# Performance work log

Hardware: AMD Instinct MI355X
Metric: run time of the kernel (lower is better)

## Reference

```python
import jax, jax.numpy as jnp
import numpy as np

B, N, IN_DIM, HID = 8, 4096, 256, 256


def setup_inputs() -> dict:
    key = jax.random.key(0)
    ks = jax.random.split(key, 7)
    s_in = 1.0 / np.sqrt(IN_DIM)
    return {
        "x": jax.random.normal(ks[0], (B, N, IN_DIM), dtype=jnp.float32),
        "Wq": jax.random.uniform(ks[1], (IN_DIM, HID), jnp.float32, -s_in, s_in),
        "bq": jax.random.uniform(ks[2], (HID,), jnp.float32, -s_in, s_in),
        "Wk": jax.random.uniform(ks[3], (IN_DIM, HID), jnp.float32, -s_in, s_in),
        "bk": jax.random.uniform(ks[4], (HID,), jnp.float32, -s_in, s_in),
        "Wv": jax.random.uniform(ks[5], (IN_DIM, HID), jnp.float32, -s_in, s_in),
        "bv": jax.random.uniform(ks[6], (HID,), jnp.float32, -s_in, s_in),
    }


def reference(x, Wq, bq, Wk, bk, Wv, bv):
    # x: [B, N, in_dim]
    Q = jnp.einsum("bnd,dh->bnh", x, Wq) + bq  # [B, N, H]
    K = jnp.einsum("bnd,dh->bnh", x, Wk) + bk
    V = jnp.einsum("bnd,dh->bnh", x, Wv) + bv
    scale = 1.0 / jnp.sqrt(jnp.asarray(K.shape[-1], dtype=x.dtype))
    scores = jnp.einsum("bqh,bkh->bqk", Q, K) * scale  # [B, N, N]
    attn = jax.nn.softmax(scores, axis=-1)
    out = jnp.einsum("bqk,bkh->bqh", attn, V)  # [B, N, H]
    return out.mean(axis=1)  # [B, H]
```

## Files before the change

kernel.cpp:

```cpp
#include <hip/hip_runtime.h>
#include <hip/hip_bf16.h>


#define NTOK 4096
#define HDIM 256
#define NBATCH 8
#define SCALE 0.0625f

typedef __attribute__((ext_vector_type(8))) short short8_t;
typedef __attribute__((ext_vector_type(16))) float f32x16;

__device__ __forceinline__ unsigned short f2bf(float f) {
    unsigned u = __float_as_uint(f);
    u += 0x7fff + ((u >> 16) & 1);
    return (unsigned short)(u >> 16);
}

#define MFMA(a, b, c) __builtin_amdgcn_mfma_f32_32x32x16_bf16(a, b, c, 0, 0, 0)

__device__ __forceinline__ void async_cp16(const void* g, void* l) {
    __builtin_amdgcn_global_load_lds((const __attribute__((address_space(1))) void*)g,
                                     (__attribute__((address_space(3))) void*)l, 16, 0, 0);
}

__device__ __forceinline__ void stage_swz(unsigned short* lds, const unsigned short* src,
                                          int row0, int dbase, int w, int l) {
#pragma unroll
    for (int i = 0; i < 4; ++i) {
        int rloc = w * 32 + i * 8 + (l >> 3);
        int u = (l & 7) ^ (l >> 3);
        const unsigned short* g = src + (size_t)(row0 + rloc) * HDIM + dbase + u * 8;
        unsigned short* d = lds + (w * 32 + i * 8) * 64;
        async_cp16(g, d);
    }
}

__device__ __forceinline__ short8_t frd(const unsigned short* lds, int rb, int lo, int u) {
    return *(const short8_t*)(lds + ((rb * 32 + lo) * 8 + (u ^ (lo & 7))) * 8);
}

__device__ __forceinline__ void stage64(unsigned short* lds, const unsigned short* src,
                                        int w, const int* soff) {
#pragma unroll
    for (int j = 0; j < 4; ++j)
        async_cp16(src + soff[j], lds + (size_t)(w * 4 + j) * 512);
}

__device__ __forceinline__ short8_t krd(const unsigned short* lds, int r, int u) {
    int dc = u >> 3, uu = u & 7;
    return *(const short8_t*)(lds + ((dc * 64 + r) * 8 + (uu ^ (r & 7))) * 8);
}

__global__ void zero_kernel(float* __restrict__ w, float* __restrict__ l, float* __restrict__ out) {
    int i = blockIdx.x * 256 + threadIdx.x;
    w[i] = 0.f;
    l[i] = 0.f;
    if (i < NBATCH * HDIM) out[i] = 0.f;
}

__global__ void convert_x(const float* __restrict__ x, unsigned short* __restrict__ xbf) {
    int i = (blockIdx.x * 256 + threadIdx.x) * 4;
    float4 v = *(const float4*)(x + i);
    ushort4 o;
    o.x = f2bf(v.x); o.y = f2bf(v.y); o.z = f2bf(v.z); o.w = f2bf(v.w);
    *(ushort4*)(xbf + i) = o;
}

__global__ void convert_wt(const float* __restrict__ Wq, const float* __restrict__ Wk,
                           const float* __restrict__ Wv, unsigned short* __restrict__ Wt) {
    int z = blockIdx.y;
    const float* W = (z == 0) ? Wq : (z == 1) ? Wk : Wv;
    unsigned short* o = Wt + z * 65536;
    int n = threadIdx.x;
    for (int kk = 0; kk < 32; ++kk) {
        int k = blockIdx.x * 32 + kk;
        o[n * 256 + k] = f2bf(W[k * 256 + n]);
    }
}

__global__ __launch_bounds__(256) void qkv_mfma(const unsigned short* __restrict__ xbf,
                                                const unsigned short* __restrict__ Wt,
                                                const float* __restrict__ bq, const float* __restrict__ bk,
                                                const float* __restrict__ bv,
                                                unsigned short* __restrict__ Qbf,
                                                unsigned short* __restrict__ Kbf,
                                                float* __restrict__ Vf) {
    const int z = blockIdx.z;
    const unsigned short* Wz = Wt + z * 65536;
    const float* bias = (z == 0) ? bq : (z == 1) ? bk : bv;
    const int m0 = blockIdx.x * 128, n0 = blockIdx.y * 128;
    const int t = threadIdx.x, w = t >> 6, l = t & 63, lo = l & 31, hi = l >> 5;
    const int rm = (w & 1) * 2, rn = (w >> 1) * 2;

    __shared__ __align__(16) char smem[32768];
    unsigned short* Xb = (unsigned short*)smem;
    unsigned short* Wb = (unsigned short*)(smem + 16384);

    f32x16 acc[2][2];
#pragma unroll
    for (int a = 0; a < 2; ++a)
#pragma unroll
        for (int c = 0; c < 2; ++c)
#pragma unroll
            for (int r = 0; r < 16; ++r) acc[a][c][r] = 0.f;

    for (int dc = 0; dc < 4; ++dc) {
        __syncthreads();
        stage_swz(Xb, xbf, m0, dc * 64, w, l);
        stage_swz(Wb, Wz, n0, dc * 64, w, l);
        __syncthreads();
#pragma unroll
        for (int ks = 0; ks < 4; ++ks) {
            int u = ks * 2 + hi;
            short8_t a0 = frd(Xb, rm + 0, lo, u);
            short8_t a1 = frd(Xb, rm + 1, lo, u);
            short8_t b0 = frd(Wb, rn + 0, lo, u);
            short8_t b1 = frd(Wb, rn + 1, lo, u);
            acc[0][0] = MFMA(a0, b0, acc[0][0]);
            acc[0][1] = MFMA(a0, b1, acc[0][1]);
            acc[1][0] = MFMA(a1, b0, acc[1][0]);
            acc[1][1] = MFMA(a1, b1, acc[1][1]);
        }
    }
    float bc0 = bias[n0 + (w >> 1) * 64 + lo];
    float bc1 = bias[n0 + (w >> 1) * 64 + 32 + lo];
#pragma unroll
    for (int mb = 0; mb < 2; ++mb)
#pragma unroll
        for (int r = 0; r < 16; ++r) {
            int row = m0 + (w & 1) * 64 + mb * 32 + (r & 3) + 8 * (r >> 2) + 4 * hi;
            int c0 = n0 + (w >> 1) * 64 + lo, c1 = c0 + 32;
            float v0 = acc[mb][0][r] + bc0;
            float v1 = acc[mb][1][r] + bc1;
            if (z == 2) {
                Vf[(size_t)row * HDIM + c0] = v0;
                Vf[(size_t)row * HDIM + c1] = v1;
            } else {
                unsigned short* o = (z == 0) ? Qbf : Kbf;
                o[(size_t)row * HDIM + c0] = f2bf(v0);
                o[(size_t)row * HDIM + c1] = f2bf(v1);
            }
        }
}

__global__ __launch_bounds__(512, 4) void score_pass1(const unsigned short* __restrict__ Qbf,
                                                      const unsigned short* __restrict__ Kbf,
                                                      float* __restrict__ lsum) {
    const int id = blockIdx.x;
    const int xcd = id & 7, j = id >> 3;
    const int qtile = j & 15, gh = j >> 4;
    const int g = xcd * 4 + gh;
    const int kslice = g & 3, b = g >> 2;

    const int q0 = qtile * 256;
    const int kbase = kslice * 1024;
    const int t = threadIdx.x, w = t >> 6, l = t & 63, lo = l & 31, hi = l >> 5;
    const unsigned short* Qb = Qbf + (size_t)b * NTOK * HDIM;
    const unsigned short* Kb = Kbf + (size_t)b * NTOK * HDIM;

    __shared__ __align__(16) unsigned short Kbuf[2][16384];

    int soff[4];
#pragma unroll
    for (int jj = 0; jj < 4; ++jj) {
        int idx = (w * 4 + jj) * 64 + l;
        int r = (idx >> 3) & 63, dc = idx >> 9;
        int u = (idx & 7) ^ (r & 7);
        soff[jj] = r * HDIM + dc * 64 + u * 8;
    }

    const unsigned short* src = Kb + (size_t)kbase * HDIM;
    stage64(Kbuf[0], src, w, soff);
    src += 64 * HDIM;

    short8_t A[16];
    const unsigned short* qrow = Qb + (size_t)(q0 + w * 32 + lo) * HDIM + hi * 8;
#pragma unroll
    for (int st = 0; st < 16; ++st) A[st] = *(const short8_t*)(qrow + st * 16);

    float rs[16];
#pragma unroll
    for (int r = 0; r < 16; ++r) rs[r] = 0.f;

    __syncthreads();

    int cur = 0;
    for (int kt = 0; kt < 16; ++kt) {
        if (kt < 15) { stage64(Kbuf[cur ^ 1], src, w, soff); src += 64 * HDIM; }
        const unsigned short* KL = Kbuf[cur];
#pragma unroll
        for (int h = 0; h < 2; ++h) {
            const int rr = h * 32 + lo;
            f32x16 acc;
#pragma unroll
            for (int r = 0; r < 16; ++r) acc[r] = 0.f;
#pragma unroll
            for (int st = 0; st < 16; ++st)
                acc = MFMA(A[st], krd(KL, rr, st * 2 + hi), acc);
#pragma unroll
            for (int r = 0; r < 16; ++r) rs[r] += __expf(acc[r] * SCALE);
        }
        __syncthreads();
        cur ^= 1;
    }

#pragma unroll
    for (int r = 0; r < 16; ++r) {
        float v = rs[r];
        v += __shfl_xor(v, 1);
        v += __shfl_xor(v, 2);
        v += __shfl_xor(v, 4);
        v += __shfl_xor(v, 8);
        v += __shfl_xor(v, 16);
        rs[r] = v;
    }
    if (lo == 0) {
#pragma unroll
        for (int r = 0; r < 16; ++r) {
            int row = q0 + w * 32 + (r & 3) + 8 * (r >> 2) + 4 * hi;
            atomicAdd(&lsum[b * NTOK + row], rs[r]);
        }
    }
}

__global__ __launch_bounds__(512, 4) void score_pass2(const unsigned short* __restrict__ Qbf,
                                                      const unsigned short* __restrict__ Kbf,
                                                      const float* __restrict__ lsum,
                                                      float* __restrict__ wsum) {
    const int id = blockIdx.x;
    const int xcd = id & 7, j = id >> 3;
    const int ktile = j & 15, gh = j >> 4;
    const int g = xcd * 4 + gh;
    const int qslice = g & 3, b = g >> 2;

    const int k0 = ktile * 256;
    const int qbase = qslice * 1024;
    const int t = threadIdx.x, w = t >> 6, l = t & 63, lo = l & 31, hi = l >> 5;
    const unsigned short* Qb = Qbf + (size_t)b * NTOK * HDIM;
    const unsigned short* Kb = Kbf + (size_t)b * NTOK * HDIM;
    const float* lb = lsum + (size_t)b * NTOK;

    __shared__ __align__(16) unsigned short Qbuf[2][16384];

    int soff[4];
#pragma unroll
    for (int jj = 0; jj < 4; ++jj) {
        int idx = (w * 4 + jj) * 64 + l;
        int r = (idx >> 3) & 63, dc = idx >> 9;
        int u = (idx & 7) ^ (r & 7);
        soff[jj] = r * HDIM + dc * 64 + u * 8;
    }

    const unsigned short* src = Qb + (size_t)qbase * HDIM;
    stage64(Qbuf[0], src, w, soff);
    src += 64 * HDIM;

    short8_t A[16];
    const unsigned short* krow = Kb + (size_t)(k0 + w * 32 + lo) * HDIM + hi * 8;
#pragma unroll
    for (int st = 0; st < 16; ++st) A[st] = *(const short8_t*)(krow + st * 16);

    float cs[16];
#pragma unroll
    for (int r = 0; r < 16; ++r) cs[r] = 0.f;

    __syncthreads();

    int cur = 0;
    for (int qt = 0; qt < 16; ++qt) {
        if (qt < 15) { stage64(Qbuf[cur ^ 1], src, w, soff); src += 64 * HDIM; }
        const unsigned short* QL = Qbuf[cur];
#pragma unroll
        for (int h = 0; h < 2; ++h) {
            const int rr = h * 32 + lo;
            float linv = 1.0f / lb[qbase + qt * 64 + rr];
            f32x16 acc;
#pragma unroll
            for (int r = 0; r < 16; ++r) acc[r] = 0.f;
#pragma unroll
            for (int st = 0; st < 16; ++st)
                acc = MFMA(A[st], krd(QL, rr, st * 2 + hi), acc);
#pragma unroll
            for (int r = 0; r < 16; ++r) cs[r] += __expf(acc[r] * SCALE) * linv;
        }
        __syncthreads();
        cur ^= 1;
    }

#pragma unroll
    for (int r = 0; r < 16; ++r) {
        float v = cs[r];
        v += __shfl_xor(v, 1);
        v += __shfl_xor(v, 2);
        v += __shfl_xor(v, 4);
        v += __shfl_xor(v, 8);
        v += __shfl_xor(v, 16);
        cs[r] = v;
    }
    if (lo == 0) {
#pragma unroll
        for (int r = 0; r < 16; ++r) {
            int row = k0 + w * 32 + (r & 3) + 8 * (r >> 2) + 4 * hi;
            atomicAdd(&wsum[b * NTOK + row], cs[r]);
        }
    }
}

__global__ __launch_bounds__(256) void finalize_kernel(const float* __restrict__ V,
                                                       const float* __restrict__ w,
                                                       float* __restrict__ out) {
    const int b = blockIdx.y;
    const int k0 = blockIdx.x * 256;
    const int h = threadIdx.x;
    __shared__ float wsh[256];
    wsh[h] = w[b * NTOK + k0 + h];
    __syncthreads();
    const float* Vb = V + ((size_t)b * NTOK + k0) * HDIM;
    float acc = 0.f;
#pragma unroll 4
    for (int kk = 0; kk < 256; ++kk) acc = fmaf(wsh[kk], Vb[(size_t)kk * HDIM + h], acc);
    atomicAdd(&out[b * HDIM + h], acc * (1.0f / (float)NTOK));
}

extern "C" void kernel_launch(void* const* d_in, const int* in_sizes, int n_in,
                              void* d_out, int out_size, void* d_ws, size_t ws_size,
                              hipStream_t stream) {
    const float* x  = (const float*)d_in[0];
    const float* Wq = (const float*)d_in[1];
    const float* bq = (const float*)d_in[2];
    const float* Wk = (const float*)d_in[3];
    const float* bk = (const float*)d_in[4];
    const float* Wv = (const float*)d_in[5];
    const float* bv = (const float*)d_in[6];
    float* out = (float*)d_out;

    const size_t BNH = (size_t)NBATCH * NTOK * HDIM;
    unsigned short* Wt  = (unsigned short*)d_ws;
    unsigned short* xbf = Wt + 3 * 65536;
    unsigned short* Qbf = xbf + BNH;
    unsigned short* Kbf = Qbf + BNH;
    float* Vf   = (float*)(Kbf + BNH);
    float* lsum = Vf + BNH;
    float* wsum = lsum + (size_t)NBATCH * NTOK;

    zero_kernel<<<dim3(128), dim3(256), 0, stream>>>(wsum, lsum, out);
    convert_x<<<dim3(8192), dim3(256), 0, stream>>>(x, xbf);
    convert_wt<<<dim3(8, 3), dim3(256), 0, stream>>>(Wq, Wk, Wv, Wt);
    qkv_mfma<<<dim3(256, 2, 3), dim3(256), 0, stream>>>(xbf, Wt, bq, bk, bv, Qbf, Kbf, Vf);
    score_pass1<<<dim3(512), dim3(512), 0, stream>>>(Qbf, Kbf, lsum);
    score_pass2<<<dim3(512), dim3(512), 0, stream>>>(Qbf, Kbf, lsum, wsum);
    finalize_kernel<<<dim3(16, 8), dim3(256), 0, stream>>>(Vf, wsum, out);
}
```

Measured before the change: 295.6 us.

## Double per-warp row tile in score passes to reuse each LDS fragment twice

Each warp in both score passes now holds two 32-row register tiles of the stationary operand (64 rows) and issues two MFMAs per LDS-loaded fragment. Block tiles grow to 512 rows and the grid halves to 256 blocks. The aim is to halve LDS reads and global K/Q staging per MFMA. In exchange, register pressure roughly doubles (launch-bounds occupancy hint dropped), and with 256 blocks the GPU's CUs hold only about one block each, so occupancy falls.

```diff
diff --git a/kernel.cpp b/kernel.cpp
--- a/kernel.cpp
+++ b/kernel.cpp
@@ -143,16 +143,16 @@
         }
 }
 
-__global__ __launch_bounds__(512, 4) void score_pass1(const unsigned short* __restrict__ Qbf,
-                                                      const unsigned short* __restrict__ Kbf,
-                                                      float* __restrict__ lsum) {
+__global__ __launch_bounds__(512) void score_pass1(const unsigned short* __restrict__ Qbf,
+                                                   const unsigned short* __restrict__ Kbf,
+                                                   float* __restrict__ lsum) {
     const int id = blockIdx.x;
     const int xcd = id & 7, j = id >> 3;
-    const int qtile = j & 15, gh = j >> 4;
+    const int qtile = j & 7, gh = j >> 3;
     const int g = xcd * 4 + gh;
     const int kslice = g & 3, b = g >> 2;
 
-    const int q0 = qtile * 256;
+    const int q0 = qtile * 512;
     const int kbase = kslice * 1024;
     const int t = threadIdx.x, w = t >> 6, l = t & 63, lo = l & 31, hi = l >> 5;
     const unsigned short* Qb = Qbf + (size_t)b * NTOK * HDIM;
@@ -173,14 +173,17 @@
     stage64(Kbuf[0], src, w, soff);
     src += 64 * HDIM;
 
-    short8_t A[16];
-    const unsigned short* qrow = Qb + (size_t)(q0 + w * 32 + lo) * HDIM + hi * 8;
-#pragma unroll
-    for (int st = 0; st < 16; ++st) A[st] = *(const short8_t*)(qrow + st * 16);
-
-    float rs[16];
-#pragma unroll
-    for (int r = 0; r < 16; ++r) rs[r] = 0.f;
+    short8_t A0[16], A1[16];
+    const unsigned short* qrow = Qb + (size_t)(q0 + w * 64 + lo) * HDIM + hi * 8;
+#pragma unroll
+    for (int st = 0; st < 16; ++st) {
+        A0[st] = *(const short8_t*)(qrow + st * 16);
+        A1[st] = *(const short8_t*)(qrow + 32 * HDIM + st * 16);
+    }
+
+    float rs0[16], rs1[16];
+#pragma unroll
+    for (int r = 0; r < 16; ++r) { rs0[r] = 0.f; rs1[r] = 0.f; }
 
     __syncthreads();
 
@@ -191,14 +194,20 @@
 #pragma unroll
         for (int h = 0; h < 2; ++h) {
             const int rr = h * 32 + lo;
-            f32x16 acc;
-#pragma unroll
-            for (int r = 0; r < 16; ++r) acc[r] = 0.f;
-#pragma unroll
-            for (int st = 0; st < 16; ++st)
-                acc = MFMA(A[st], krd(KL, rr, st * 2 + hi), acc);
-#pragma unroll
-            for (int r = 0; r < 16; ++r) rs[r] += __expf(acc[r] * SCALE);
+            f32x16 acc0, acc1;
+#pragma unroll
+            for (int r = 0; r < 16; ++r) { acc0[r] = 0.f; acc1[r] = 0.f; }
+#pragma unroll
+            for (int st = 0; st < 16; ++st) {
+                short8_t bb = krd(KL, rr, st * 2 + hi);
+                acc0 = MFMA(A0[st], bb, acc0);
+                acc1 = MFMA(A1[st], bb, acc1);
+            }
+#pragma unroll
+            for (int r = 0; r < 16; ++r) {
+                rs0[r] += __expf(acc0[r] * SCALE);
+                rs1[r] += __expf(acc1[r] * SCALE);
+            }
         }
         __syncthreads();
         cur ^= 1;
@@ -206,34 +215,35 @@
 
 #pragma unroll
     for (int r = 0; r < 16; ++r) {
-        float v = rs[r];
-        v += __shfl_xor(v, 1);
-        v += __shfl_xor(v, 2);
-        v += __shfl_xor(v, 4);
-        v += __shfl_xor(v, 8);
-        v += __shfl_xor(v, 16);
-        rs[r] = v;
+        float v0 = rs0[r], v1 = rs1[r];
+        v0 += __shfl_xor(v0, 1);  v1 += __shfl_xor(v1, 1);
+        v0 += __shfl_xor(v0, 2);  v1 += __shfl_xor(v1, 2);
+        v0 += __shfl_xor(v0, 4);  v1 += __shfl_xor(v1, 4);
+        v0 += __shfl_xor(v0, 8);  v1 += __shfl_xor(v1, 8);
+        v0 += __shfl_xor(v0, 16); v1 += __shfl_xor(v1, 16);
+        rs0[r] = v0; rs1[r] = v1;
     }
     if (lo == 0) {
 #pragma unroll
         for (int r = 0; r < 16; ++r) {
-            int row = q0 + w * 32 + (r & 3) + 8 * (r >> 2) + 4 * hi;
-            atomicAdd(&lsum[b * NTOK + row], rs[r]);
-        }
-    }
-}
-
-__global__ __launch_bounds__(512, 4) void score_pass2(const unsigned short* __restrict__ Qbf,
-                                                      const unsigned short* __restrict__ Kbf,
-                                                      const float* __restrict__ lsum,
-                                                      float* __restrict__ wsum) {
+            int rmap = (r & 3) + 8 * (r >> 2) + 4 * hi;
+            atomicAdd(&lsum[b * NTOK + q0 + w * 64 + rmap], rs0[r]);
+            atomicAdd(&lsum[b * NTOK + q0 + w * 64 + 32 + rmap], rs1[r]);
+        }
+    }
+}
+
+__global__ __launch_bounds__(512) void score_pass2(const unsigned short* __restrict__ Qbf,
+                                                   const unsigned short* __restrict__ Kbf,
+                                                   const float* __restrict__ lsum,
+                                                   float* __restrict__ wsum) {
     const int id = blockIdx.x;
     const int xcd = id & 7, j = id >> 3;
-    const int ktile = j & 15, gh = j >> 4;
+    const int ktile = j & 7, gh = j >> 3;
     const int g = xcd * 4 + gh;
     const int qslice = g & 3, b = g >> 2;
 
-    const int k0 = ktile * 256;
+    const int k0 = ktile * 512;
     const int qbase = qslice * 1024;
     const int t = threadIdx.x, w = t >> 6, l = t & 63, lo = l & 31, hi = l >> 5;
     const unsigned short* Qb = Qbf + (size_t)b * NTOK * HDIM;
@@ -255,14 +265,17 @@
     stage64(Qbuf[0], src, w, soff);
     src += 64 * HDIM;
 
-    short8_t A[16];
-    const unsigned short* krow = Kb + (size_t)(k0 + w * 32 + lo) * HDIM + hi * 8;
-#pragma unroll
-    for (int st = 0; st < 16; ++st) A[st] = *(const short8_t*)(krow + st * 16);
-
-    float cs[16];
-#pragma unroll
-    for (int r = 0; r < 16; ++r) cs[r] = 0.f;
+    short8_t A0[16], A1[16];
+    const unsigned short* krow = Kb + (size_t)(k0 + w * 64 + lo) * HDIM + hi * 8;
+#pragma unroll
+    for (int st = 0; st < 16; ++st) {
+        A0[st] = *(const short8_t*)(krow + st * 16);
+        A1[st] = *(const short8_t*)(krow + 32 * HDIM + st * 16);
+    }
+
+    float cs0[16], cs1[16];
+#pragma unroll
+    for (int r = 0; r < 16; ++r) { cs0[r] = 0.f; cs1[r] = 0.f; }
 
     __syncthreads();
 
@@ -274,14 +287,20 @@
         for (int h = 0; h < 2; ++h) {
             const int rr = h * 32 + lo;
             float linv = 1.0f / lb[qbase + qt * 64 + rr];
-            f32x16 acc;
-#pragma unroll
-            for (int r = 0; r < 16; ++r) acc[r] = 0.f;
-#pragma unroll
-            for (int st = 0; st < 16; ++st)
-                acc = MFMA(A[st], krd(QL, rr, st * 2 + hi), acc);
-#pragma unroll
-            for (int r = 0; r < 16; ++r) cs[r] += __expf(acc[r] * SCALE) * linv;
+            f32x16 acc0, acc1;
+#pragma unroll
+            for (int r = 0; r < 16; ++r) { acc0[r] = 0.f; acc1[r] = 0.f; }
+#pragma unroll
+            for (int st = 0; st < 16; ++st) {
+                short8_t bb = krd(QL, rr, st * 2 + hi);
+                acc0 = MFMA(A0[st], bb, acc0);
+                acc1 = MFMA(A1[st], bb, acc1);
+            }
+#pragma unroll
+            for (int r = 0; r < 16; ++r) {
+                cs0[r] += __expf(acc0[r] * SCALE) * linv;
+                cs1[r] += __expf(acc1[r] * SCALE) * linv;
+            }
         }
         __syncthreads();
         cur ^= 1;
@@ -289,19 +308,20 @@
 
 #pragma unroll
     for (int r = 0; r < 16; ++r) {
-        float v = cs[r];
-        v += __shfl_xor(v, 1);
-        v += __shfl_xor(v, 2);
-        v += __shfl_xor(v, 4);
-        v += __shfl_xor(v, 8);
-        v += __shfl_xor(v, 16);
-        cs[r] = v;
+        float v0 = cs0[r], v1 = cs1[r];
+        v0 += __shfl_xor(v0, 1);  v1 += __shfl_xor(v1, 1);
+        v0 += __shfl_xor(v0, 2);  v1 += __shfl_xor(v1, 2);
+        v0 += __shfl_xor(v0, 4);  v1 += __shfl_xor(v1, 4);
+        v0 += __shfl_xor(v0, 8);  v1 += __shfl_xor(v1, 8);
+        v0 += __shfl_xor(v0, 16); v1 += __shfl_xor(v1, 16);
+        cs0[r] = v0; cs1[r] = v1;
     }
     if (lo == 0) {
 #pragma unroll
         for (int r = 0; r < 16; ++r) {
-            int row = k0 + w * 32 + (r & 3) + 8 * (r >> 2) + 4 * hi;
-            atomicAdd(&wsum[b * NTOK + row], cs[r]);
+            int rmap = (r & 3) + 8 * (r >> 2) + 4 * hi;
+            atomicAdd(&wsum[b * NTOK + k0 + w * 64 + rmap], cs0[r]);
+            atomicAdd(&wsum[b * NTOK + k0 + w * 64 + 32 + rmap], cs1[r]);
         }
     }
 }
@@ -347,7 +367,7 @@
     convert_x<<<dim3(8192), dim3(256), 0, stream>>>(x, xbf);
     convert_wt<<<dim3(8, 3), dim3(256), 0, stream>>>(Wq, Wk, Wv, Wt);
     qkv_mfma<<<dim3(256, 2, 3), dim3(256), 0, stream>>>(xbf, Wt, bq, bk, bv, Qbf, Kbf, Vf);
-    score_pass1<<<dim3(512), dim3(512), 0, stream>>>(Qbf, Kbf, lsum);
-    score_pass2<<<dim3(512), dim3(512), 0, stream>>>(Qbf, Kbf, lsum, wsum);
+    score_pass1<<<dim3(256), dim3(512), 0, stream>>>(Qbf, Kbf, lsum);
+    score_pass2<<<dim3(256), dim3(512), 0, stream>>>(Qbf, Kbf, lsum, wsum);
     finalize_kernel<<<dim3(16, 8), dim3(256), 0, stream>>>(Vf, wsum, out);
 }
```

Result: faster. 283.6 us (-4.1%).

## Retile score passes to 128-row tiles with waves splitting key halves

Applied to the files above, without the earlier changes.

Both score passes now give each block a 128-row query (or key) tile over a 2048-long slice instead of a 256-row tile over 1024. Eight waves are split into four row sets times two halves of each staged 64-row tile, so each wave runs one 32x32 MFMA chain per stage instead of two. Staged K/Q tiles are shared across waves in the same way, but each block now streams twice as many stages and the min-blocks occupancy hint is dropped. The intent is to cut per-wave work per barrier and change register pressure, at the cost of more LDS staging per output row.

```diff
diff --git a/kernel.cpp b/kernel.cpp
--- a/kernel.cpp
+++ b/kernel.cpp
@@ -143,18 +143,19 @@
         }
 }
 
-__global__ __launch_bounds__(512, 4) void score_pass1(const unsigned short* __restrict__ Qbf,
-                                                      const unsigned short* __restrict__ Kbf,
-                                                      float* __restrict__ lsum) {
+__global__ __launch_bounds__(512) void score_pass1(const unsigned short* __restrict__ Qbf,
+                                                   const unsigned short* __restrict__ Kbf,
+                                                   float* __restrict__ lsum) {
     const int id = blockIdx.x;
     const int xcd = id & 7, j = id >> 3;
-    const int qtile = j & 15, gh = j >> 4;
-    const int g = xcd * 4 + gh;
-    const int kslice = g & 3, b = g >> 2;
-
-    const int q0 = qtile * 256;
-    const int kbase = kslice * 1024;
+    const int qtile = j & 31, gh = j >> 5;
+    const int g = xcd * 2 + gh;
+    const int kslice = g & 1, b = g >> 1;
+
+    const int q0 = qtile * 128;
+    const int kbase = kslice * 2048;
     const int t = threadIdx.x, w = t >> 6, l = t & 63, lo = l & 31, hi = l >> 5;
+    const int qset = w & 3, khalf = w >> 2;
     const unsigned short* Qb = Qbf + (size_t)b * NTOK * HDIM;
     const unsigned short* Kb = Kbf + (size_t)b * NTOK * HDIM;
 
@@ -174,7 +175,7 @@
     src += 64 * HDIM;
 
     short8_t A[16];
-    const unsigned short* qrow = Qb + (size_t)(q0 + w * 32 + lo) * HDIM + hi * 8;
+    const unsigned short* qrow = Qb + (size_t)(q0 + qset * 32 + lo) * HDIM + hi * 8;
 #pragma unroll
     for (int st = 0; st < 16; ++st) A[st] = *(const short8_t*)(qrow + st * 16);
 
@@ -184,22 +185,17 @@
 
     __syncthreads();
 
+    const int rr = khalf * 32 + lo;
     int cur = 0;
-    for (int kt = 0; kt < 16; ++kt) {
-        if (kt < 15) { stage64(Kbuf[cur ^ 1], src, w, soff); src += 64 * HDIM; }
+    for (int kt = 0; kt < 32; ++kt) {
+        if (kt < 31) { stage64(Kbuf[cur ^ 1], src, w, soff); src += 64 * HDIM; }
         const unsigned short* KL = Kbuf[cur];
-#pragma unroll
-        for (int h = 0; h < 2; ++h) {
-            const int rr = h * 32 + lo;
-            f32x16 acc;
-#pragma unroll
-            for (int r = 0; r < 16; ++r) acc[r] = 0.f;
-#pragma unroll
-            for (int st = 0; st < 16; ++st)
-                acc = MFMA(A[st], krd(KL, rr, st * 2 + hi), acc);
-#pragma unroll
-            for (int r = 0; r < 16; ++r) rs[r] += __expf(acc[r] * SCALE);
-        }
+        f32x16 acc = {};
+#pragma unroll
+        for (int st = 0; st < 16; ++st)
+            acc = MFMA(A[st], krd(KL, rr, st * 2 + hi), acc);
+#pragma unroll
+        for (int r = 0; r < 16; ++r) rs[r] += __expf(acc[r] * SCALE);
         __syncthreads();
         cur ^= 1;
     }
@@ -217,25 +213,26 @@
     if (lo == 0) {
 #pragma unroll
         for (int r = 0; r < 16; ++r) {
-            int row = q0 + w * 32 + (r & 3) + 8 * (r >> 2) + 4 * hi;
+            int row = q0 + qset * 32 + (r & 3) + 8 * (r >> 2) + 4 * hi;
             atomicAdd(&lsum[b * NTOK + row], rs[r]);
         }
     }
 }
 
-__global__ __launch_bounds__(512, 4) void score_pass2(const unsigned short* __restrict__ Qbf,
-                                                      const unsigned short* __restrict__ Kbf,
-                                                      const float* __restrict__ lsum,
-                                                      float* __restrict__ wsum) {
+__global__ __launch_bounds__(512) void score_pass2(const unsigned short* __restrict__ Qbf,
+                                                   const unsigned short* __restrict__ Kbf,
+                                                   const float* __restrict__ lsum,
+                                                   float* __restrict__ wsum) {
     const int id = blockIdx.x;
     const int xcd = id & 7, j = id >> 3;
-    const int ktile = j & 15, gh = j >> 4;
-    const int g = xcd * 4 + gh;
-    const int qslice = g & 3, b = g >> 2;
-
-    const int k0 = ktile * 256;
-    const int qbase = qslice * 1024;
+    const int ktile = j & 31, gh = j >> 5;
+    const int g = xcd * 2 + gh;
+    const int qslice = g & 1, b = g >> 1;
+
+    const int k0 = ktile * 128;
+    const int qbase = qslice * 2048;
     const int t = threadIdx.x, w = t >> 6, l = t & 63, lo = l & 31, hi = l >> 5;
+    const int kset = w & 3, qhalf = w >> 2;
     const unsigned short* Qb = Qbf + (size_t)b * NTOK * HDIM;
     const unsigned short* Kb = Kbf + (size_t)b * NTOK * HDIM;
     const float* lb = lsum + (size_t)b * NTOK;
@@ -256,7 +253,7 @@
     src += 64 * HDIM;
 
     short8_t A[16];
-    const unsigned short* krow = Kb + (size_t)(k0 + w * 32 + lo) * HDIM + hi * 8;
+    const unsigned short* krow = Kb + (size_t)(k0 + kset * 32 + lo) * HDIM + hi * 8;
 #pragma unroll
     for (int st = 0; st < 16; ++st) A[st] = *(const short8_t*)(krow + st * 16);
 
@@ -266,23 +263,18 @@
 
     __syncthreads();
 
+    const int rr = qhalf * 32 + lo;
     int cur = 0;
-    for (int qt = 0; qt < 16; ++qt) {
-        if (qt < 15) { stage64(Qbuf[cur ^ 1], src, w, soff); src += 64 * HDIM; }
+    for (int qt = 0; qt < 32; ++qt) {
+        if (qt < 31) { stage64(Qbuf[cur ^ 1], src, w, soff); src += 64 * HDIM; }
+        float linv = 1.0f / lb[qbase + qt * 64 + rr];
         const unsigned short* QL = Qbuf[cur];
-#pragma unroll
-        for (int h = 0; h < 2; ++h) {
-            const int rr = h * 32 + lo;
-            float linv = 1.0f / lb[qbase + qt * 64 + rr];
-            f32x16 acc;
-#pragma unroll
-            for (int r = 0; r < 16; ++r) acc[r] = 0.f;
-#pragma unroll
-            for (int st = 0; st < 16; ++st)
-                acc = MFMA(A[st], krd(QL, rr, st * 2 + hi), acc);
-#pragma unroll
-            for (int r = 0; r < 16; ++r) cs[r] += __expf(acc[r] * SCALE) * linv;
-        }
+        f32x16 acc = {};
+#pragma unroll
+        for (int st = 0; st < 16; ++st)
+            acc = MFMA(A[st], krd(QL, rr, st * 2 + hi), acc);
+#pragma unroll
+        for (int r = 0; r < 16; ++r) cs[r] += __expf(acc[r] * SCALE) * linv;
         __syncthreads();
         cur ^= 1;
     }
@@ -300,7 +292,7 @@
     if (lo == 0) {
 #pragma unroll
         for (int r = 0; r < 16; ++r) {
-            int row = k0 + w * 32 + (r & 3) + 8 * (r >> 2) + 4 * hi;
+            int row = k0 + kset * 32 + (r & 3) + 8 * (r >> 2) + 4 * hi;
             atomicAdd(&wsum[b * NTOK + row], cs[r]);
         }
     }
```

After: 288.9 us. 1.02x faster.
